# Kernel optimization log

Hardware: AMD Instinct MI355X
Metric: run time of the kernel (lower is better)

## Reference

```python
import jax, jax.numpy as jnp
import numpy as np

B, S, D, H = 4, 2048, 1024, 16
DK = D // H

def setup_inputs() -> dict:
    key = jax.random.key(0)
    ks = jax.random.split(key, 11)
    s = 1.0 / np.sqrt(D)
    return {
        "query": jax.random.normal(ks[0], (B, S, D), jnp.float32),
        "key": jax.random.normal(ks[1], (B, S, D), jnp.float32),
        "value": jax.random.normal(ks[2], (B, S, D), jnp.float32),
        "Wq_w": jax.random.normal(ks[3], (D, D), jnp.float32) * s,
        "Wq_b": jnp.zeros((D,), jnp.float32),
        "Wk_w": jax.random.normal(ks[4], (D, D), jnp.float32) * s,
        "Wk_b": jnp.zeros((D,), jnp.float32),
        "Wv_w": jax.random.normal(ks[5], (D, D), jnp.float32) * s,
        "Wv_b": jnp.zeros((D,), jnp.float32),
        "Wo_w": jax.random.normal(ks[6], (D, D), jnp.float32) * s,
        "Wo_b": jnp.zeros((D,), jnp.float32),
    }

def reference(query, key, value, Wq_w, Wq_b, Wk_w, Wk_b, Wv_w, Wv_b, Wo_w, Wo_b):
    b, s, d = query.shape
    # Linear projections (torch Linear: x @ W.T + b)
    q = query @ Wq_w.T + Wq_b
    k = key @ Wk_w.T + Wk_b
    v = value @ Wv_w.T + Wv_b
    # split heads -> [B, H, S, DK]
    q = q.reshape(b, s, H, DK).transpose(0, 2, 1, 3)
    k = k.reshape(b, s, H, DK).transpose(0, 2, 1, 3)
    v = v.reshape(b, s, H, DK).transpose(0, 2, 1, 3)
    # scaled dot-product attention
    scores = jnp.einsum("bhqd,bhkd->bhqk", q, k) / jnp.sqrt(jnp.asarray(DK, q.dtype))
    attn = jax.nn.softmax(scores, axis=-1)
    z = jnp.einsum("bhqk,bhkd->bhqd", attn, v)
    # merge heads and output projection
    z = z.transpose(0, 2, 1, 3).reshape(b, s, H * DK)
    return z @ Wo_w.T + Wo_b
```

## Files before the change

### kernel.cpp

```cpp
#include <hip/hip_runtime.h>
#include <stdint.h>

typedef unsigned short u16;
typedef __bf16 bf16x8 __attribute__((ext_vector_type(8)));
typedef float f32x4 __attribute__((ext_vector_type(4)));

#define B_   4
#define S_   2048
#define D_   1024
#define H_   16
#define DK_  64
#define MTOK (B_*S_)
#define LOG2E 1.4426950408889634f

static __device__ __forceinline__ float exp2_fast(float x){
  return __builtin_amdgcn_exp2f(x);
}

static __device__ __forceinline__ void gload_lds16(const void* g, void* l){
  __builtin_amdgcn_global_load_lds(
      (const __attribute__((address_space(1))) unsigned int*)g,
      (__attribute__((address_space(3))) unsigned int*)l, 16, 0, 0);
}

union bf8pack { __bf16 h[8]; uint4 u; };

__global__ void cvt4(const float* __restrict__ s0, const float* __restrict__ s1,
                     const float* __restrict__ s2, const float* __restrict__ s3,
                     u16* __restrict__ out, int n8){
  const float* s = blockIdx.y==0 ? s0 : blockIdx.y==1 ? s1 : blockIdx.y==2 ? s2 : s3;
  u16* o = out + (size_t)blockIdx.y * ((size_t)n8 * 8);
  int i = blockIdx.x * blockDim.x + threadIdx.x;
  int stride = gridDim.x * blockDim.x;
  for (; i < n8; i += stride){
    float4 v0 = reinterpret_cast<const float4*>(s)[i*2];
    float4 v1 = reinterpret_cast<const float4*>(s)[i*2+1];
    bf8pack p;
    p.h[0]=(__bf16)v0.x; p.h[1]=(__bf16)v0.y; p.h[2]=(__bf16)v0.z; p.h[3]=(__bf16)v0.w;
    p.h[4]=(__bf16)v1.x; p.h[5]=(__bf16)v1.y; p.h[6]=(__bf16)v1.z; p.h[7]=(__bf16)v1.w;
    reinterpret_cast<uint4*>(o)[i] = p.u;
  }
}

__global__ __launch_bounds__(256) void gemm_qkv(
    const float* __restrict__ q_in, const float* __restrict__ k_in, const float* __restrict__ v_in,
    const u16* __restrict__ wq, const u16* __restrict__ wk, const u16* __restrict__ wv,
    const float* __restrict__ bq, const float* __restrict__ bk, const float* __restrict__ bv,
    u16* __restrict__ Qb, u16* __restrict__ Kb, u16* __restrict__ VtG){
  const int z = blockIdx.z;
  const float* Ap   = z==0 ? q_in : z==1 ? k_in : v_in;
  const u16*   Bw   = z==0 ? wq : z==1 ? wk : wv;
  const float* bias = z==0 ? bq : z==1 ? bk : bv;
  const float scale = z==0 ? 0.125f*LOG2E : 1.0f;
  u16* Cb = z==0 ? Qb : z==1 ? Kb : VtG;

  __shared__ u16 As[128][32];
  __shared__ u16 Bs[128][32];
  const int tid  = threadIdx.x;
  const int lane = tid & 63;
  const int wid  = tid >> 6;
  const int wr = wid >> 1, wc = wid & 1;
  const int r15 = lane & 15, q4 = lane >> 4;
  const int bm = blockIdx.x, bn = blockIdx.y;
  const int K = D_, N = D_;

  f32x4 acc[4][4] = {};

  for (int kt = 0; kt < K; kt += 32){
    #pragma unroll
    for (int i = 0; i < 2; ++i){
      int c = i*256 + tid;
      int row = c >> 2, col = (c & 3) << 3;
      const float* Af = Ap + (size_t)(bm*128 + row)*K + kt + col;
      float4 v0 = *reinterpret_cast<const float4*>(Af);
      float4 v1 = *reinterpret_cast<const float4*>(Af + 4);
      bf8pack p;
      p.h[0]=(__bf16)v0.x; p.h[1]=(__bf16)v0.y; p.h[2]=(__bf16)v0.z; p.h[3]=(__bf16)v0.w;
      p.h[4]=(__bf16)v1.x; p.h[5]=(__bf16)v1.y; p.h[6]=(__bf16)v1.z; p.h[7]=(__bf16)v1.w;
      *reinterpret_cast<uint4*>(&As[row][col]) = p.u;
      gload_lds16(Bw + (size_t)(bn*128 + row)*K + kt + col, &Bs[row][col]);
    }
    __syncthreads();

    bf16x8 af[4], bfr[4];
    #pragma unroll
    for (int mf = 0; mf < 4; ++mf)
      af[mf] = *reinterpret_cast<const bf16x8*>(&As[wr*64 + mf*16 + r15][q4*8]);
    #pragma unroll
    for (int nf = 0; nf < 4; ++nf)
      bfr[nf] = *reinterpret_cast<const bf16x8*>(&Bs[wc*64 + nf*16 + r15][q4*8]);
    #pragma unroll
    for (int mf = 0; mf < 4; ++mf)
      #pragma unroll
      for (int nf = 0; nf < 4; ++nf)
        acc[mf][nf] = __builtin_amdgcn_mfma_f32_16x16x32_bf16(af[mf], bfr[nf], acc[mf][nf], 0, 0, 0);
    __syncthreads();
  }

  #pragma unroll
  for (int nf = 0; nf < 4; ++nf){
    int col = bn*128 + wc*64 + nf*16 + r15;
    float bv = bias[col];
    if (z == 2){
      int h = col >> 6, dk = col & 63;
      #pragma unroll
      for (int mf = 0; mf < 4; ++mf){
        int row0 = bm*128 + wr*64 + mf*16 + q4*4;
        int bb = row0 >> 11, s0 = row0 & (S_-1);
        bf8pack p;
        #pragma unroll
        for (int j = 0; j < 4; ++j) p.h[j] = (__bf16)(acc[mf][nf][j] + bv);
        uint2 u; u.x = p.u.x; u.y = p.u.y;
        *reinterpret_cast<uint2*>(&Cb[((size_t)(bb*H_ + h)*DK_ + dk)*S_ + s0]) = u;
      }
    } else {
      #pragma unroll
      for (int mf = 0; mf < 4; ++mf){
        #pragma unroll
        for (int j = 0; j < 4; ++j){
          int row = bm*128 + wr*64 + mf*16 + q4*4 + j;
          __bf16 hv = (__bf16)((acc[mf][nf][j] + bv) * scale);
          Cb[(size_t)row*N + col] = *reinterpret_cast<u16*>(&hv);
        }
      }
    }
  }
}

__global__ __launch_bounds__(256) void gemm_out(const u16* __restrict__ Ab,
    const u16* __restrict__ Bw, const float* __restrict__ bias, float* __restrict__ Cf){
  __shared__ u16 As[128][32];
  __shared__ u16 Bs[128][32];
  const int tid  = threadIdx.x;
  const int lane = tid & 63;
  const int wid  = tid >> 6;
  const int wr = wid >> 1, wc = wid & 1;
  const int r15 = lane & 15, q4 = lane >> 4;
  const int bm = blockIdx.x, bn = blockIdx.y;
  const int K = D_, N = D_;

  f32x4 acc[4][4] = {};

  for (int kt = 0; kt < K; kt += 32){
    #pragma unroll
    for (int i = 0; i < 2; ++i){
      int c = i*256 + tid;
      int row = c >> 2, col = (c & 3) << 3;
      gload_lds16(Ab + (size_t)(bm*128 + row)*K + kt + col, &As[row][col]);
      gload_lds16(Bw + (size_t)(bn*128 + row)*K + kt + col, &Bs[row][col]);
    }
    __syncthreads();

    bf16x8 af[4], bfr[4];
    #pragma unroll
    for (int mf = 0; mf < 4; ++mf)
      af[mf] = *reinterpret_cast<const bf16x8*>(&As[wr*64 + mf*16 + r15][q4*8]);
    #pragma unroll
    for (int nf = 0; nf < 4; ++nf)
      bfr[nf] = *reinterpret_cast<const bf16x8*>(&Bs[wc*64 + nf*16 + r15][q4*8]);
    #pragma unroll
    for (int mf = 0; mf < 4; ++mf)
      #pragma unroll
      for (int nf = 0; nf < 4; ++nf)
        acc[mf][nf] = __builtin_amdgcn_mfma_f32_16x16x32_bf16(af[mf], bfr[nf], acc[mf][nf], 0, 0, 0);
    __syncthreads();
  }

  #pragma unroll
  for (int nf = 0; nf < 4; ++nf){
    int col = bn*128 + wc*64 + nf*16 + r15;
    float bv = bias[col];
    #pragma unroll
    for (int mf = 0; mf < 4; ++mf)
      #pragma unroll
      for (int j = 0; j < 4; ++j){
        int row = bm*128 + wr*64 + mf*16 + q4*4 + j;
        Cf[(size_t)row*N + col] = acc[mf][nf][j] + bv;
      }
  }
}

__global__ __launch_bounds__(256) void attn128(const u16* __restrict__ Qg,
    const u16* __restrict__ Kg, const u16* __restrict__ VtG, u16* __restrict__ Zg){
  __shared__ u16 Ks[64][72];
  __shared__ u16 Vts[64][72];
  __shared__ __bf16 Ps[128][68];
  const int tid  = threadIdx.x;
  const int lane = tid & 63;
  const int wv   = tid >> 6;
  const int r15  = lane & 15, q4 = lane >> 4;
  const int qt = blockIdx.x;
  const int bh = blockIdx.y;
  const int b = bh >> 4, h = bh & (H_-1);
  const size_t baseQ = ((size_t)b * S_) * D_ + (size_t)h * DK_;
  const size_t baseV = (size_t)bh * DK_ * S_;
  const int q0 = qt * 128;

  bf16x8 aq[2][2];
  #pragma unroll
  for (int mf = 0; mf < 2; ++mf){
    const u16* qr = Qg + baseQ + (size_t)(q0 + wv*32 + mf*16 + r15) * D_;
    aq[mf][0] = *reinterpret_cast<const bf16x8*>(qr + q4*8);
    aq[mf][1] = *reinterpret_cast<const bf16x8*>(qr + 32 + q4*8);
  }

  bf16x8 vones;
  #pragma unroll
  for (int i = 0; i < 8; ++i) vones[i] = (__bf16)1.0f;

  const int srow = tid >> 3, scol = (tid & 7) << 3;
  const u16* Kbase = Kg + baseQ;
  const u16* Vbase = VtG + baseV;

  uint4 kreg0, kreg1, vreg0, vreg1;
  kreg0 = *reinterpret_cast<const uint4*>(Kbase + (size_t)srow*D_ + scol);
  kreg1 = *reinterpret_cast<const uint4*>(Kbase + (size_t)(srow+32)*D_ + scol);
  vreg0 = *reinterpret_cast<const uint4*>(Vbase + (size_t)srow*S_ + scol);
  vreg1 = *reinterpret_cast<const uint4*>(Vbase + (size_t)(srow+32)*S_ + scol);

  f32x4 o_acc[2][4] = {};
  f32x4 l_acc[2] = {};

  for (int kt = 0; kt < S_/64; ++kt){
    if (kt) __syncthreads();
    *reinterpret_cast<uint4*>(&Ks[srow][scol])      = kreg0;
    *reinterpret_cast<uint4*>(&Ks[srow+32][scol])   = kreg1;
    *reinterpret_cast<uint4*>(&Vts[srow][scol])     = vreg0;
    *reinterpret_cast<uint4*>(&Vts[srow+32][scol])  = vreg1;
    __syncthreads();

    if (kt + 1 < S_/64){
      const u16* kp = Kbase + (size_t)((kt+1)*64 + srow)*D_ + scol;
      kreg0 = *reinterpret_cast<const uint4*>(kp);
      kreg1 = *reinterpret_cast<const uint4*>(kp + (size_t)32*D_);
      const u16* vp = Vbase + (size_t)srow*S_ + (kt+1)*64 + scol;
      vreg0 = *reinterpret_cast<const uint4*>(vp);
      vreg1 = *reinterpret_cast<const uint4*>(vp + (size_t)32*S_);
    }

    bf16x8 bk[4][2];
    #pragma unroll
    for (int nf = 0; nf < 4; ++nf){
      bk[nf][0] = *reinterpret_cast<const bf16x8*>(&Ks[nf*16 + r15][q4*8]);
      bk[nf][1] = *reinterpret_cast<const bf16x8*>(&Ks[nf*16 + r15][32 + q4*8]);
    }

    #pragma unroll
    for (int mf = 0; mf < 2; ++mf){
      f32x4 sacc[4] = {};
      #pragma unroll
      for (int nf = 0; nf < 4; ++nf){
        sacc[nf] = __builtin_amdgcn_mfma_f32_16x16x32_bf16(aq[mf][0], bk[nf][0], sacc[nf], 0, 0, 0);
        sacc[nf] = __builtin_amdgcn_mfma_f32_16x16x32_bf16(aq[mf][1], bk[nf][1], sacc[nf], 0, 0, 0);
      }
      #pragma unroll
      for (int nf = 0; nf < 4; ++nf)
        #pragma unroll
        for (int j = 0; j < 4; ++j)
          Ps[wv*32 + mf*16 + q4*4 + j][nf*16 + r15] = (__bf16)exp2_fast(sacc[nf][j]);
    }

    #pragma unroll
    for (int ks = 0; ks < 2; ++ks){
      bf16x8 bvf[4];
      #pragma unroll
      for (int nf = 0; nf < 4; ++nf)
        bvf[nf] = *reinterpret_cast<const bf16x8*>(&Vts[nf*16 + r15][ks*32 + q4*8]);
      #pragma unroll
      for (int mf = 0; mf < 2; ++mf){
        uint2 plo = *reinterpret_cast<const uint2*>(&Ps[wv*32 + mf*16 + r15][ks*32 + q4*8]);
        uint2 phi = *reinterpret_cast<const uint2*>(&Ps[wv*32 + mf*16 + r15][ks*32 + q4*8 + 4]);
        uint4 pw; pw.x = plo.x; pw.y = plo.y; pw.z = phi.x; pw.w = phi.y;
        bf16x8 ap = *reinterpret_cast<bf16x8*>(&pw);
        #pragma unroll
        for (int nf = 0; nf < 4; ++nf)
          o_acc[mf][nf] = __builtin_amdgcn_mfma_f32_16x16x32_bf16(ap, bvf[nf], o_acc[mf][nf], 0, 0, 0);
        l_acc[mf] = __builtin_amdgcn_mfma_f32_16x16x32_bf16(ap, vones, l_acc[mf], 0, 0, 0);
      }
    }
  }

  #pragma unroll
  for (int mf = 0; mf < 2; ++mf){
    f32x4 inv;
    #pragma unroll
    for (int j = 0; j < 4; ++j) inv[j] = 1.0f / l_acc[mf][j];
    #pragma unroll
    for (int nf = 0; nf < 4; ++nf)
      #pragma unroll
      for (int j = 0; j < 4; ++j){
        int qrw = q0 + wv*32 + mf*16 + q4*4 + j;
        int col = nf*16 + r15;
        __bf16 hv = (__bf16)(o_acc[mf][nf][j] * inv[j]);
        Zg[baseQ + (size_t)qrw*D_ + col] = *reinterpret_cast<u16*>(&hv);
      }
  }
}

extern "C" void kernel_launch(void* const* d_in, const int* in_sizes, int n_in,
                              void* d_out, int out_size, void* d_ws, size_t ws_size,
                              hipStream_t stream){
  const float* q_in = (const float*)d_in[0];
  const float* k_in = (const float*)d_in[1];
  const float* v_in = (const float*)d_in[2];
  const float* Wq_w = (const float*)d_in[3];
  const float* Wq_b = (const float*)d_in[4];
  const float* Wk_w = (const float*)d_in[5];
  const float* Wk_b = (const float*)d_in[6];
  const float* Wv_w = (const float*)d_in[7];
  const float* Wv_b = (const float*)d_in[8];
  const float* Wo_w = (const float*)d_in[9];
  const float* Wo_b = (const float*)d_in[10];
  float* out = (float*)d_out;

  u16* ws = (u16*)d_ws;
  const size_t WE = (size_t)D_ * D_;
  const size_t XE = (size_t)MTOK * D_;
  u16* wqb = ws;
  u16* wkb = wqb + WE;
  u16* wvb = wkb + WE;
  u16* wob = wvb + WE;
  u16* Qb  = wob + WE;
  u16* Kb  = Qb + XE;
  u16* VtG = Kb + XE;
  u16* Zb  = VtG + XE;

  cvt4<<<dim3(128, 4), 256, 0, stream>>>(Wq_w, Wk_w, Wv_w, Wo_w, wqb, (int)(WE/8));

  dim3 gqkv(MTOK/128, D_/128, 3), bb(256);
  gemm_qkv<<<gqkv, bb, 0, stream>>>(q_in, k_in, v_in, wqb, wkb, wvb,
                                    Wq_b, Wk_b, Wv_b, Qb, Kb, VtG);

  attn128<<<dim3(S_/128, B_*H_), bb, 0, stream>>>(Qb, Kb, VtG, Zb);

  gemm_out<<<dim3(MTOK/128, D_/128), bb, 0, stream>>>(Zb, wob, Wo_b, out);
}
```

Baseline: 240.7 us.

## Double-buffer LDS tiles in QKV and output projection GEMMs

Both projection GEMMs now use two LDS buffers per operand. The next K-tile is prefetched (global loads, plus the fp32-to-bf16 conversion for the activation input in the QKV GEMM) while MFMAs run on the current tile, which removes one barrier per iteration. The aim is to hide global memory latency behind compute. In exchange, LDS use doubles and register pressure rises from the held prefetch values, which may reduce occupancy.

```diff
diff --git a/kernel.cpp b/kernel.cpp
--- a/kernel.cpp
+++ b/kernel.cpp
@@ -54,8 +54,8 @@
   const float scale = z==0 ? 0.125f*LOG2E : 1.0f;
   u16* Cb = z==0 ? Qb : z==1 ? Kb : VtG;
 
-  __shared__ u16 As[128][32];
-  __shared__ u16 Bs[128][32];
+  __shared__ u16 As[2][128][32];
+  __shared__ u16 Bs[2][128][32];
   const int tid  = threadIdx.x;
   const int lane = tid & 63;
   const int wid  = tid >> 6;
@@ -63,37 +63,70 @@
   const int r15 = lane & 15, q4 = lane >> 4;
   const int bm = blockIdx.x, bn = blockIdx.y;
   const int K = D_, N = D_;
+  const int NT = K / 32;
+
+  const int r = tid >> 2, c = (tid & 3) << 3;
+  const float* Ar0 = Ap + (size_t)(bm*128 + r)*K + c;
+  const float* Ar1 = Ap + (size_t)(bm*128 + r + 64)*K + c;
+  const u16*  Br0 = Bw + (size_t)(bn*128 + r)*K + c;
+  const u16*  Br1 = Bw + (size_t)(bn*128 + r + 64)*K + c;
 
   f32x4 acc[4][4] = {};
 
-  for (int kt = 0; kt < K; kt += 32){
-    #pragma unroll
-    for (int i = 0; i < 2; ++i){
-      int c = i*256 + tid;
-      int row = c >> 2, col = (c & 3) << 3;
-      const float* Af = Ap + (size_t)(bm*128 + row)*K + kt + col;
-      float4 v0 = *reinterpret_cast<const float4*>(Af);
-      float4 v1 = *reinterpret_cast<const float4*>(Af + 4);
-      bf8pack p;
-      p.h[0]=(__bf16)v0.x; p.h[1]=(__bf16)v0.y; p.h[2]=(__bf16)v0.z; p.h[3]=(__bf16)v0.w;
-      p.h[4]=(__bf16)v1.x; p.h[5]=(__bf16)v1.y; p.h[6]=(__bf16)v1.z; p.h[7]=(__bf16)v1.w;
-      *reinterpret_cast<uint4*>(&As[row][col]) = p.u;
-      gload_lds16(Bw + (size_t)(bn*128 + row)*K + kt + col, &Bs[row][col]);
-    }
-    __syncthreads();
+  {
+    float4 v00 = *reinterpret_cast<const float4*>(Ar0);
+    float4 v01 = *reinterpret_cast<const float4*>(Ar0 + 4);
+    float4 v10 = *reinterpret_cast<const float4*>(Ar1);
+    float4 v11 = *reinterpret_cast<const float4*>(Ar1 + 4);
+    bf8pack p0, p1;
+    p0.h[0]=(__bf16)v00.x; p0.h[1]=(__bf16)v00.y; p0.h[2]=(__bf16)v00.z; p0.h[3]=(__bf16)v00.w;
+    p0.h[4]=(__bf16)v01.x; p0.h[5]=(__bf16)v01.y; p0.h[6]=(__bf16)v01.z; p0.h[7]=(__bf16)v01.w;
+    p1.h[0]=(__bf16)v10.x; p1.h[1]=(__bf16)v10.y; p1.h[2]=(__bf16)v10.z; p1.h[3]=(__bf16)v10.w;
+    p1.h[4]=(__bf16)v11.x; p1.h[5]=(__bf16)v11.y; p1.h[6]=(__bf16)v11.z; p1.h[7]=(__bf16)v11.w;
+    *reinterpret_cast<uint4*>(&As[0][r][c])    = p0.u;
+    *reinterpret_cast<uint4*>(&As[0][r+64][c]) = p1.u;
+    gload_lds16(Br0, &Bs[0][r][c]);
+    gload_lds16(Br1, &Bs[0][r+64][c]);
+  }
+  __syncthreads();
+
+  for (int t = 0; t < NT; ++t){
+    const int cur = t & 1;
+    float4 v00, v01, v10, v11;
+    const bool pf = (t + 1 < NT);
+    if (pf){
+      const float* p0 = Ar0 + (t+1)*32;
+      const float* p1 = Ar1 + (t+1)*32;
+      v00 = *reinterpret_cast<const float4*>(p0);
+      v01 = *reinterpret_cast<const float4*>(p0 + 4);
+      v10 = *reinterpret_cast<const float4*>(p1);
+      v11 = *reinterpret_cast<const float4*>(p1 + 4);
+      gload_lds16(Br0 + (t+1)*32, &Bs[cur^1][r][c]);
+      gload_lds16(Br1 + (t+1)*32, &Bs[cur^1][r+64][c]);
+    }
 
     bf16x8 af[4], bfr[4];
     #pragma unroll
     for (int mf = 0; mf < 4; ++mf)
-      af[mf] = *reinterpret_cast<const bf16x8*>(&As[wr*64 + mf*16 + r15][q4*8]);
+      af[mf] = *reinterpret_cast<const bf16x8*>(&As[cur][wr*64 + mf*16 + r15][q4*8]);
     #pragma unroll
     for (int nf = 0; nf < 4; ++nf)
-      bfr[nf] = *reinterpret_cast<const bf16x8*>(&Bs[wc*64 + nf*16 + r15][q4*8]);
+      bfr[nf] = *reinterpret_cast<const bf16x8*>(&Bs[cur][wc*64 + nf*16 + r15][q4*8]);
     #pragma unroll
     for (int mf = 0; mf < 4; ++mf)
       #pragma unroll
       for (int nf = 0; nf < 4; ++nf)
         acc[mf][nf] = __builtin_amdgcn_mfma_f32_16x16x32_bf16(af[mf], bfr[nf], acc[mf][nf], 0, 0, 0);
+
+    if (pf){
+      bf8pack p0, p1;
+      p0.h[0]=(__bf16)v00.x; p0.h[1]=(__bf16)v00.y; p0.h[2]=(__bf16)v00.z; p0.h[3]=(__bf16)v00.w;
+      p0.h[4]=(__bf16)v01.x; p0.h[5]=(__bf16)v01.y; p0.h[6]=(__bf16)v01.z; p0.h[7]=(__bf16)v01.w;
+      p1.h[0]=(__bf16)v10.x; p1.h[1]=(__bf16)v10.y; p1.h[2]=(__bf16)v10.z; p1.h[3]=(__bf16)v10.w;
+      p1.h[4]=(__bf16)v11.x; p1.h[5]=(__bf16)v11.y; p1.h[6]=(__bf16)v11.z; p1.h[7]=(__bf16)v11.w;
+      *reinterpret_cast<uint4*>(&As[cur^1][r][c])    = p0.u;
+      *reinterpret_cast<uint4*>(&As[cur^1][r+64][c]) = p1.u;
+    }
     __syncthreads();
   }
 
@@ -129,8 +162,8 @@
 
 __global__ __launch_bounds__(256) void gemm_out(const u16* __restrict__ Ab,
     const u16* __restrict__ Bw, const float* __restrict__ bias, float* __restrict__ Cf){
-  __shared__ u16 As[128][32];
-  __shared__ u16 Bs[128][32];
+  __shared__ u16 As[2][128][32];
+  __shared__ u16 Bs[2][128][32];
   const int tid  = threadIdx.x;
   const int lane = tid & 63;
   const int wid  = tid >> 6;
@@ -138,26 +171,38 @@
   const int r15 = lane & 15, q4 = lane >> 4;
   const int bm = blockIdx.x, bn = blockIdx.y;
   const int K = D_, N = D_;
+  const int NT = K / 32;
+
+  const int r = tid >> 2, c = (tid & 3) << 3;
+  const u16* Ar0 = Ab + (size_t)(bm*128 + r)*K + c;
+  const u16* Ar1 = Ab + (size_t)(bm*128 + r + 64)*K + c;
+  const u16* Br0 = Bw + (size_t)(bn*128 + r)*K + c;
+  const u16* Br1 = Bw + (size_t)(bn*128 + r + 64)*K + c;
 
   f32x4 acc[4][4] = {};
 
-  for (int kt = 0; kt < K; kt += 32){
-    #pragma unroll
-    for (int i = 0; i < 2; ++i){
-      int c = i*256 + tid;
-      int row = c >> 2, col = (c & 3) << 3;
-      gload_lds16(Ab + (size_t)(bm*128 + row)*K + kt + col, &As[row][col]);
-      gload_lds16(Bw + (size_t)(bn*128 + row)*K + kt + col, &Bs[row][col]);
-    }
-    __syncthreads();
+  gload_lds16(Ar0, &As[0][r][c]);
+  gload_lds16(Ar1, &As[0][r+64][c]);
+  gload_lds16(Br0, &Bs[0][r][c]);
+  gload_lds16(Br1, &Bs[0][r+64][c]);
+  __syncthreads();
+
+  for (int t = 0; t < NT; ++t){
+    const int cur = t & 1;
+    if (t + 1 < NT){
+      gload_lds16(Ar0 + (t+1)*32, &As[cur^1][r][c]);
+      gload_lds16(Ar1 + (t+1)*32, &As[cur^1][r+64][c]);
+      gload_lds16(Br0 + (t+1)*32, &Bs[cur^1][r][c]);
+      gload_lds16(Br1 + (t+1)*32, &Bs[cur^1][r+64][c]);
+    }
 
     bf16x8 af[4], bfr[4];
     #pragma unroll
     for (int mf = 0; mf < 4; ++mf)
-      af[mf] = *reinterpret_cast<const bf16x8*>(&As[wr*64 + mf*16 + r15][q4*8]);
+      af[mf] = *reinterpret_cast<const bf16x8*>(&As[cur][wr*64 + mf*16 + r15][q4*8]);
     #pragma unroll
     for (int nf = 0; nf < 4; ++nf)
-      bfr[nf] = *reinterpret_cast<const bf16x8*>(&Bs[wc*64 + nf*16 + r15][q4*8]);
+      bfr[nf] = *reinterpret_cast<const bf16x8*>(&Bs[cur][wc*64 + nf*16 + r15][q4*8]);
     #pragma unroll
     for (int mf = 0; mf < 4; ++mf)
       #pragma unroll
```

Result: faster. 224.1 us, median of 2 (-6.9%).

## Double-buffer QKV and output GEMMs with async LDS prefetch and XCD-aware attention grid

Applied to the files above, without the earlier changes.

Both projection GEMMs now keep LDS tiles in multiple buffers. The next tile's global loads (register-staged fp32 A with bf16 packing in gemm_qkv, direct-to-LDS loads in gemm_out) are issued before computing on the current tile, and one waitcnt+barrier per step replaces the two __syncthreads. The goal is to hide global memory latency behind MFMA work. The attention launch becomes a 1D grid remapped so each XCD handles a contiguous set of (batch, head) pairs, which should improve L2 reuse of K/V. In exchange the GEMMs use more LDS and registers, and the hand-written vmcnt counts must match exactly.

```diff
diff --git a/kernel.cpp b/kernel.cpp
--- a/kernel.cpp
+++ b/kernel.cpp
@@ -24,6 +24,25 @@
 }
 
 union bf8pack { __bf16 h[8]; uint4 u; };
+
+#define WSYNC(N) { \
+  asm volatile("s_waitcnt vmcnt(" #N ") lgkmcnt(0)" ::: "memory"); \
+  __builtin_amdgcn_s_barrier(); \
+  __builtin_amdgcn_sched_barrier(0); }
+
+#define COMPUTE(ASBUF, BSBUF) { \
+  bf16x8 af_[4], bf_[4]; \
+  _Pragma("unroll") \
+  for (int mf_ = 0; mf_ < 4; ++mf_) \
+    af_[mf_] = *reinterpret_cast<const bf16x8*>(&As[ASBUF][wr*64 + mf_*16 + r15][q4*8]); \
+  _Pragma("unroll") \
+  for (int nf_ = 0; nf_ < 4; ++nf_) \
+    bf_[nf_] = *reinterpret_cast<const bf16x8*>(&Bs[BSBUF][wc*64 + nf_*16 + r15][q4*8]); \
+  _Pragma("unroll") \
+  for (int mf_ = 0; mf_ < 4; ++mf_) \
+    _Pragma("unroll") \
+    for (int nf_ = 0; nf_ < 4; ++nf_) \
+      acc[mf_][nf_] = __builtin_amdgcn_mfma_f32_16x16x32_bf16(af_[mf_], bf_[nf_], acc[mf_][nf_], 0, 0, 0); }
 
 __global__ void cvt4(const float* __restrict__ s0, const float* __restrict__ s1,
                      const float* __restrict__ s2, const float* __restrict__ s3,
@@ -42,6 +61,27 @@
   }
 }
 
+#define LOADA(P, T) { \
+  const float* pA0_ = Ab0 + (size_t)(T)*32; \
+  const float* pA1_ = Ab1 + (size_t)(T)*32; \
+  P[0] = *reinterpret_cast<const float4*>(pA0_); \
+  P[1] = *reinterpret_cast<const float4*>(pA0_ + 4); \
+  P[2] = *reinterpret_cast<const float4*>(pA1_); \
+  P[3] = *reinterpret_cast<const float4*>(pA1_ + 4); }
+
+#define PACKA(P, BUF) { \
+  bf8pack pk0_, pk1_; \
+  pk0_.h[0]=(__bf16)P[0].x; pk0_.h[1]=(__bf16)P[0].y; pk0_.h[2]=(__bf16)P[0].z; pk0_.h[3]=(__bf16)P[0].w; \
+  pk0_.h[4]=(__bf16)P[1].x; pk0_.h[5]=(__bf16)P[1].y; pk0_.h[6]=(__bf16)P[1].z; pk0_.h[7]=(__bf16)P[1].w; \
+  pk1_.h[0]=(__bf16)P[2].x; pk1_.h[1]=(__bf16)P[2].y; pk1_.h[2]=(__bf16)P[2].z; pk1_.h[3]=(__bf16)P[2].w; \
+  pk1_.h[4]=(__bf16)P[3].x; pk1_.h[5]=(__bf16)P[3].y; pk1_.h[6]=(__bf16)P[3].z; pk1_.h[7]=(__bf16)P[3].w; \
+  *reinterpret_cast<uint4*>(&As[BUF][r][c])    = pk0_.u; \
+  *reinterpret_cast<uint4*>(&As[BUF][r+64][c]) = pk1_.u; }
+
+#define GLOADB(T, BUF) { \
+  gload_lds16(Bb0 + (size_t)(T)*32, &Bs[BUF][r][c]); \
+  gload_lds16(Bb1 + (size_t)(T)*32, &Bs[BUF][r+64][c]); }
+
 __global__ __launch_bounds__(256) void gemm_qkv(
     const float* __restrict__ q_in, const float* __restrict__ k_in, const float* __restrict__ v_in,
     const u16* __restrict__ wq, const u16* __restrict__ wk, const u16* __restrict__ wv,
@@ -54,8 +94,8 @@
   const float scale = z==0 ? 0.125f*LOG2E : 1.0f;
   u16* Cb = z==0 ? Qb : z==1 ? Kb : VtG;
 
-  __shared__ u16 As[128][32];
-  __shared__ u16 Bs[128][32];
+  __shared__ u16 As[2][128][32];
+  __shared__ u16 Bs[2][128][32];
   const int tid  = threadIdx.x;
   const int lane = tid & 63;
   const int wid  = tid >> 6;
@@ -63,38 +103,31 @@
   const int r15 = lane & 15, q4 = lane >> 4;
   const int bm = blockIdx.x, bn = blockIdx.y;
   const int K = D_, N = D_;
+  const int NT = 32;
+
+  const int r = tid >> 2, c = (tid & 3) << 3;
+  const float* Ab0 = Ap + (size_t)(bm*128 + r)*K + c;
+  const float* Ab1 = Ap + (size_t)(bm*128 + r + 64)*K + c;
+  const u16*  Bb0 = Bw + (size_t)(bn*128 + r)*K + c;
+  const u16*  Bb1 = Bw + (size_t)(bn*128 + r + 64)*K + c;
 
   f32x4 acc[4][4] = {};
-
-  for (int kt = 0; kt < K; kt += 32){
-    #pragma unroll
-    for (int i = 0; i < 2; ++i){
-      int c = i*256 + tid;
-      int row = c >> 2, col = (c & 3) << 3;
-      const float* Af = Ap + (size_t)(bm*128 + row)*K + kt + col;
-      float4 v0 = *reinterpret_cast<const float4*>(Af);
-      float4 v1 = *reinterpret_cast<const float4*>(Af + 4);
-      bf8pack p;
-      p.h[0]=(__bf16)v0.x; p.h[1]=(__bf16)v0.y; p.h[2]=(__bf16)v0.z; p.h[3]=(__bf16)v0.w;
-      p.h[4]=(__bf16)v1.x; p.h[5]=(__bf16)v1.y; p.h[6]=(__bf16)v1.z; p.h[7]=(__bf16)v1.w;
-      *reinterpret_cast<uint4*>(&As[row][col]) = p.u;
-      gload_lds16(Bw + (size_t)(bn*128 + row)*K + kt + col, &Bs[row][col]);
-    }
-    __syncthreads();
-
-    bf16x8 af[4], bfr[4];
-    #pragma unroll
-    for (int mf = 0; mf < 4; ++mf)
-      af[mf] = *reinterpret_cast<const bf16x8*>(&As[wr*64 + mf*16 + r15][q4*8]);
-    #pragma unroll
-    for (int nf = 0; nf < 4; ++nf)
-      bfr[nf] = *reinterpret_cast<const bf16x8*>(&Bs[wc*64 + nf*16 + r15][q4*8]);
-    #pragma unroll
-    for (int mf = 0; mf < 4; ++mf)
-      #pragma unroll
-      for (int nf = 0; nf < 4; ++nf)
-        acc[mf][nf] = __builtin_amdgcn_mfma_f32_16x16x32_bf16(af[mf], bfr[nf], acc[mf][nf], 0, 0, 0);
-    __syncthreads();
+  float4 sA[4], sB[4];
+
+  LOADA(sA, 0); GLOADB(0, 0); PACKA(sA, 0); LOADA(sA, 1);
+  WSYNC(4)
+
+  for (int t = 0; t < NT; t += 2){
+    if (t+1 < NT) GLOADB(t+1, 1)
+    if (t+2 < NT) LOADA(sB, t+2)
+    COMPUTE(0, 0)
+    if (t+1 < NT) PACKA(sA, 1)
+    if (t+2 < NT) { WSYNC(4) } else { WSYNC(0) }
+    if (t+2 < NT) GLOADB(t+2, 0)
+    if (t+3 < NT) LOADA(sA, t+3)
+    COMPUTE(1, 1)
+    if (t+2 < NT) PACKA(sB, 0)
+    if (t+3 < NT) { WSYNC(4) } else { WSYNC(0) }
   }
 
   #pragma unroll
@@ -106,12 +139,12 @@
       #pragma unroll
       for (int mf = 0; mf < 4; ++mf){
         int row0 = bm*128 + wr*64 + mf*16 + q4*4;
-        int bb = row0 >> 11, s0 = row0 & (S_-1);
+        int bb = row0 >> 11, sx = row0 & (S_-1);
         bf8pack p;
         #pragma unroll
         for (int j = 0; j < 4; ++j) p.h[j] = (__bf16)(acc[mf][nf][j] + bv);
         uint2 u; u.x = p.u.x; u.y = p.u.y;
-        *reinterpret_cast<uint2*>(&Cb[((size_t)(bb*H_ + h)*DK_ + dk)*S_ + s0]) = u;
+        *reinterpret_cast<uint2*>(&Cb[((size_t)(bb*H_ + h)*DK_ + dk)*S_ + sx]) = u;
       }
     } else {
       #pragma unroll
@@ -127,10 +160,22 @@
   }
 }
 
+#define GO_GLA(T, BUF) { \
+  gload_lds16(Aa0 + (size_t)(T)*32, &As[BUF][r][c]); \
+  gload_lds16(Aa1 + (size_t)(T)*32, &As[BUF][r+64][c]); }
+#define GO_GLB(T, BUF) { \
+  gload_lds16(Bb0 + (size_t)(T)*32, &Bs[BUF][r][c]); \
+  gload_lds16(Bb1 + (size_t)(T)*32, &Bs[BUF][r+64][c]); }
+#define GO_BODY(T, BA, BB) { \
+  if ((T)+1 < 32) GO_GLB((T)+1, ((BB)^1)) \
+  if ((T)+2 < 32) GO_GLA((T)+2, (((BA)+2)&3)) \
+  COMPUTE(BA, BB) \
+  if ((T)+2 < 32) { WSYNC(2) } else { WSYNC(0) } }
+
 __global__ __launch_bounds__(256) void gemm_out(const u16* __restrict__ Ab,
     const u16* __restrict__ Bw, const float* __restrict__ bias, float* __restrict__ Cf){
-  __shared__ u16 As[128][32];
-  __shared__ u16 Bs[128][32];
+  __shared__ u16 As[4][128][32];
+  __shared__ u16 Bs[2][128][32];
   const int tid  = threadIdx.x;
   const int lane = tid & 63;
   const int wid  = tid >> 6;
@@ -139,31 +184,22 @@
   const int bm = blockIdx.x, bn = blockIdx.y;
   const int K = D_, N = D_;
 
+  const int r = tid >> 2, c = (tid & 3) << 3;
+  const u16* Aa0 = Ab + (size_t)(bm*128 + r)*K + c;
+  const u16* Aa1 = Ab + (size_t)(bm*128 + r + 64)*K + c;
+  const u16* Bb0 = Bw + (size_t)(bn*128 + r)*K + c;
+  const u16* Bb1 = Bw + (size_t)(bn*128 + r + 64)*K + c;
+
   f32x4 acc[4][4] = {};
 
-  for (int kt = 0; kt < K; kt += 32){
-    #pragma unroll
-    for (int i = 0; i < 2; ++i){
-      int c = i*256 + tid;
-      int row = c >> 2, col = (c & 3) << 3;
-      gload_lds16(Ab + (size_t)(bm*128 + row)*K + kt + col, &As[row][col]);
-      gload_lds16(Bw + (size_t)(bn*128 + row)*K + kt + col, &Bs[row][col]);
-    }
-    __syncthreads();
-
-    bf16x8 af[4], bfr[4];
-    #pragma unroll
-    for (int mf = 0; mf < 4; ++mf)
-      af[mf] = *reinterpret_cast<const bf16x8*>(&As[wr*64 + mf*16 + r15][q4*8]);
-    #pragma unroll
-    for (int nf = 0; nf < 4; ++nf)
-      bfr[nf] = *reinterpret_cast<const bf16x8*>(&Bs[wc*64 + nf*16 + r15][q4*8]);
-    #pragma unroll
-    for (int mf = 0; mf < 4; ++mf)
-      #pragma unroll
-      for (int nf = 0; nf < 4; ++nf)
-        acc[mf][nf] = __builtin_amdgcn_mfma_f32_16x16x32_bf16(af[mf], bfr[nf], acc[mf][nf], 0, 0, 0);
-    __syncthreads();
+  GO_GLA(0, 0) GO_GLB(0, 0) GO_GLA(1, 1)
+  WSYNC(2)
+
+  for (int t = 0; t < 32; t += 4){
+    GO_BODY(t+0, 0, 0)
+    GO_BODY(t+1, 1, 1)
+    GO_BODY(t+2, 2, 0)
+    GO_BODY(t+3, 3, 1)
   }
 
   #pragma unroll
@@ -189,8 +225,10 @@
   const int lane = tid & 63;
   const int wv   = tid >> 6;
   const int r15  = lane & 15, q4 = lane >> 4;
-  const int qt = blockIdx.x;
-  const int bh = blockIdx.y;
+  const int bid = blockIdx.x;
+  const int xcd = bid & 7, ii = bid >> 3;
+  const int bh = xcd*8 + (ii >> 4);
+  const int qt = ii & 15;
   const int b = bh >> 4, h = bh & (H_-1);
   const size_t baseQ = ((size_t)b * S_) * D_ + (size_t)h * DK_;
   const size_t baseV = (size_t)bh * DK_ * S_;
@@ -331,7 +369,7 @@
   gemm_qkv<<<gqkv, bb, 0, stream>>>(q_in, k_in, v_in, wqb, wkb, wvb,
                                     Wq_b, Wk_b, Wv_b, Qb, Kb, VtG);
 
-  attn128<<<dim3(S_/128, B_*H_), bb, 0, stream>>>(Qb, Kb, VtG, Zb);
+  attn128<<<dim3(B_*H_*(S_/128)), bb, 0, stream>>>(Qb, Kb, VtG, Zb);
 
   gemm_out<<<dim3(MTOK/128, D_/128), bb, 0, stream>>>(Zb, wob, Wo_b, out);
 }
```

Result: faster. 230.9 us (-4.1%).
